# Kernel optimization log

Hardware: AMD Instinct MI355X
Metric: run time of the kernel (lower is better)

## Reference

```python
import jax, jax.numpy as jnp
import numpy as np

B, N, E, H = 4, 8192, 256, 8
EXP = 4  # params['num_layers'] -> MLP expansion
HID = EXP * E
EPS = 1e-5


def _layernorm(x, w, b):
    mu = jnp.mean(x, axis=-1, keepdims=True)
    var = jnp.mean(jnp.square(x - mu), axis=-1, keepdims=True)
    return (x - mu) * jax.lax.rsqrt(var + EPS) * w + b


def _mish(x):
    return x * jnp.tanh(jax.nn.softplus(x))


def setup_inputs() -> dict:
    key = jax.random.key(0)
    ks = jax.random.split(key, 12)
    s = 0.02
    return {
        "x": jax.random.normal(ks[0], (B, N, E), dtype=jnp.float32),
        "ln1_w": jnp.ones((E,), jnp.float32),
        "ln1_b": jnp.zeros((E,), jnp.float32),
        "Wq": jax.random.normal(ks[1], (E, E), jnp.float32) * s,
        "bq": jnp.zeros((E,), jnp.float32),
        "Wk": jax.random.normal(ks[2], (E, E), jnp.float32) * s,
        "bk": jnp.zeros((E,), jnp.float32),
        "Wv": jax.random.normal(ks[3], (E, E), jnp.float32) * s,
        "bv": jnp.zeros((E,), jnp.float32),
        "Wp": jax.random.normal(ks[4], (E, E), jnp.float32) * s,
        "bp": jnp.zeros((E,), jnp.float32),
        "ln2_w": jnp.ones((E,), jnp.float32),
        "ln2_b": jnp.zeros((E,), jnp.float32),
        "W1": jax.random.normal(ks[5], (HID, E), jnp.float32) * s,
        "b1": jnp.zeros((HID,), jnp.float32),
        "W2": jax.random.normal(ks[6], (E, HID), jnp.float32) * s,
        "b2": jnp.zeros((E,), jnp.float32),
    }


def _msa(x, Wq, bq, Wk, bk, Wv, bv, Wp, bp):
    b, n, e = x.shape
    d = n // H  # sequence-chunk per head (faithful to source rearrange)
    q = (x @ Wq.T + bq).reshape(b, H, d, e)
    k = (x @ Wk.T + bk).reshape(b, H, d, e)
    v = (x @ Wv.T + bv).reshape(b, H, d, e)
    scale = jnp.sqrt(jnp.float32(E))
    energy = jnp.einsum('bhie,bhke->bhik', q, k)  # (b,H,d,d)
    att = jax.nn.softmax(energy, axis=3) / scale
    o = jnp.einsum('bhik,bhke->bhie', att, v).reshape(b, n, e)
    return o @ Wp.T + bp


def reference(x, ln1_w, ln1_b, Wq, bq, Wk, bk, Wv, bv, Wp, bp,
              ln2_w, ln2_b, W1, b1, W2, b2):
    # pre-LN attention block + residual
    x1 = _msa(_layernorm(x, ln1_w, ln1_b), Wq, bq, Wk, bk, Wv, bv, Wp, bp) + x
    # pre-LN MLP (Mish after both linears, per source) + residual
    h = _layernorm(x1, ln2_w, ln2_b)
    h = _mish(h @ W1.T + b1)
    h = _mish(h @ W2.T + b2)
    return h + x1
```

## Files before the change

kernel.cpp:

```cpp
#include <hip/hip_runtime.h>

typedef float  f32x4  __attribute__((ext_vector_type(4)));
typedef float  f4v    __attribute__((ext_vector_type(4)));
typedef __bf16 bf16x8 __attribute__((ext_vector_type(8)));
typedef __bf16 bf16x4 __attribute__((ext_vector_type(4)));
typedef unsigned short ushort_t;

#define AS1 __attribute__((address_space(1)))
#define AS3 __attribute__((address_space(3)))

static __device__ __forceinline__ void gload_lds16(const void* g, void* l) {
  __builtin_amdgcn_global_load_lds((const AS1 void*)g, (AS3 void*)l, 16, 0, 0);
}

static __device__ __forceinline__ float mishf(float x) {
  float t = __expf(x);
  float u = t * (t + 2.f);
  float y = x * __fdividef(u, u + 2.f);
  return (x > 15.f) ? x : y;
}

__global__ __launch_bounds__(256) void packw(
    const float* __restrict__ Wq, const float* __restrict__ Wk,
    const float* __restrict__ Wv, const float* __restrict__ Wp,
    const float* __restrict__ W1, const float* __restrict__ W2,
    __bf16* __restrict__ out)
{
  const int t = blockIdx.x * 256 + threadIdx.x;
  const int e0 = t * 8;
  int rel, K; const float* src;
  if      (e0 < 196608) { rel = e0;          K = 256;  src = nullptr; }
  else if (e0 < 262144) { rel = e0 - 196608; K = 256;  src = Wp; }
  else if (e0 < 524288) { rel = e0 - 262144; K = 256;  src = W1; }
  else                  { rel = e0 - 524288; K = 1024; src = W2; }
  const int percb = (K >> 8) * 8192;
  const int cb = rel / percb;  const int r1 = rel % percb;
  const int c  = r1 / 8192;    const int r2 = r1 % 8192;
  const int u  = r2 / 1024;    const int r3 = r2 % 1024;
  const int n  = r3 / 512;     const int l  = (r3 % 512) >> 3;
  const int col = cb * 32 + n * 16 + (l & 15);
  const int k   = c * 256 + u * 32 + ((l >> 4) << 3);
  const float* sp;
  if (e0 < 196608) {
    const float* qkvsrc = (col < 256) ? Wq : (col < 512 ? Wk : Wv);
    sp = qkvsrc + (size_t)(col & 255) * 256 + k;
  } else {
    sp = src + (size_t)col * K + k;
  }
  const f4v a = *(const f4v*)(sp);
  const f4v b = *(const f4v*)(sp + 4);
  bf16x8 o;
  #pragma unroll
  for (int j = 0; j < 4; ++j) { o[j] = (__bf16)a[j]; o[4 + j] = (__bf16)b[j]; }
  *(bf16x8*)(out + e0) = o;
}

__global__ void packb(const float* __restrict__ a, const float* __restrict__ b,
                      const float* __restrict__ c, float* __restrict__ o) {
  int i = threadIdx.x;
  o[i] = (i < 256) ? a[i] : (i < 512 ? b[i - 256] : c[i - 512]);
}

__global__ __launch_bounds__(256) void ln_rows(
    const float* __restrict__ X, const float* __restrict__ g,
    const float* __restrict__ b, __bf16* __restrict__ Y)
{
  const int l = threadIdx.x & 63;
  const size_t row = (size_t)blockIdx.x * 4 + (threadIdx.x >> 6);
  const f4v x = *(const f4v*)(X + row * 256 + l * 4);
  float s = x[0] + x[1] + x[2] + x[3];
  float q = x[0]*x[0] + x[1]*x[1] + x[2]*x[2] + x[3]*x[3];
  #pragma unroll
  for (int d = 1; d < 64; d <<= 1) { s += __shfl_xor(s, d); q += __shfl_xor(q, d); }
  const float mu = s * (1.f / 256.f);
  const float rs = rsqrtf(q * (1.f / 256.f) - mu * mu + 1e-5f);
  const f4v gv = *(const f4v*)(g + l * 4);
  const f4v bv = *(const f4v*)(b + l * 4);
  bf16x4 o;
  #pragma unroll
  for (int j = 0; j < 4; ++j) o[j] = (__bf16)((x[j] - mu) * rs * gv[j] + bv[j]);
  *(bf16x4*)(Y + row * 256 + l * 4) = o;
}

template<int BM, int NT, int KC, int ACT, int RES, int OUTBF>
__global__ __launch_bounds__(512, 2) void bgemm(
    const __bf16* __restrict__ A, const __bf16* __restrict__ Wg,
    const float* __restrict__ bias, const float* __restrict__ res,
    void* __restrict__ out, int ldo)
{
  constexpr int K  = KC * 256;
  constexpr int MR = BM / 32;
  __shared__ __bf16 Ab[BM * 256];
  const int tid = threadIdx.x, l = tid & 63, w = tid >> 6;
  const int wr = w >> 2, wc = w & 3;
  constexpr int nwg = (32768 / BM) * NT;
  const int wg = (blockIdx.x & 7) * (nwg / 8) + (blockIdx.x >> 3);
  const int mt = wg / NT, nt = wg % NT;
  const int row0 = mt * BM;
  const int col0 = nt * 256 + wc * 64;
  const int cb0 = nt * 8 + wc * 2;

  auto stageA = [&](int c) {
    #pragma unroll
    for (int j = 0; j < BM / 16; ++j) {
      const int s = j * 512 + tid;
      const int r = s >> 5, q = s & 31;
      gload_lds16(A + (size_t)(row0 + r) * K + c * 256 + ((q ^ (r & 7)) << 3),
                  &Ab[s << 3]);
    }
  };

  auto ldBu = [&](bf16x8* d, int c, int u) {
    const __bf16* wp0 = Wg + ((size_t)cb0 * KC + c) * 8192 + (((u << 1) * 64 + l) << 3);
    const __bf16* wp1 = wp0 + (size_t)KC * 8192;
    d[0] = *(const bf16x8*)(wp0);
    d[1] = *(const bf16x8*)(wp0 + 512);
    d[2] = *(const bf16x8*)(wp1);
    d[3] = *(const bf16x8*)(wp1 + 512);
  };

  f32x4 acc[MR][4] = {};

  stageA(0);
  asm volatile("s_waitcnt vmcnt(0)" ::: "memory");
  __builtin_amdgcn_s_barrier();

  for (int c = 0;;) {
    bf16x8 b0[4], b1[4];
    ldBu(b0, c, 0);
    #pragma unroll
    for (int u = 0; u < 8; ++u) {
      if (u + 1 < 8) ldBu((u & 1) ? b0 : b1, c, u + 1);
      const bf16x8* bu = (u & 1) ? b1 : b0;
      bf16x8 af[MR];
      #pragma unroll
      for (int m = 0; m < MR; ++m) {
        const int r = wr * (BM / 2) + m * 16 + (l & 15);
        const int q = ((u << 2) | (l >> 4)) ^ (r & 7);
        af[m] = *(const bf16x8*)&Ab[((r << 5) | q) << 3];
      }
      #pragma unroll
      for (int m = 0; m < MR; ++m)
        #pragma unroll
        for (int n = 0; n < 4; ++n)
          acc[m][n] = __builtin_amdgcn_mfma_f32_16x16x32_bf16(af[m], bu[n], acc[m][n], 0, 0, 0);
    }
    if (++c == KC) break;
    __syncthreads();
    stageA(c);
    asm volatile("s_waitcnt vmcnt(0)" ::: "memory");
    __builtin_amdgcn_s_barrier();
  }

  float bs[4];
  #pragma unroll
  for (int n = 0; n < 4; ++n) bs[n] = bias[col0 + n * 16 + (l & 15)];
  #pragma unroll
  for (int m = 0; m < MR; ++m) {
    #pragma unroll
    for (int r = 0; r < 4; ++r) {
      const int row = row0 + wr * (BM / 2) + m * 16 + ((l >> 4) << 2) + r;
      float v[4];
      #pragma unroll
      for (int n = 0; n < 4; ++n) {
        v[n] = acc[m][n][r] + bs[n];
        if (ACT) v[n] = mishf(v[n]);
      }
      if (OUTBF) {
        __bf16* op = (__bf16*)out + (size_t)row * ldo + col0;
        #pragma unroll
        for (int n = 0; n < 4; ++n) op[n * 16 + (l & 15)] = (__bf16)v[n];
      } else {
        float* op = (float*)out + (size_t)row * ldo + col0;
        if (RES) {
          const float* rp = res + (size_t)row * ldo + col0;
          #pragma unroll
          for (int n = 0; n < 4; ++n) v[n] += rp[n * 16 + (l & 15)];
        }
        #pragma unroll
        for (int n = 0; n < 4; ++n) op[n * 16 + (l & 15)] = v[n];
      }
    }
  }
}

__global__ __launch_bounds__(512) void attn_fwd(
    const __bf16* __restrict__ QKV, __bf16* __restrict__ Om)
{
  __shared__ __bf16 Ks[2][32][256];
  __shared__ __bf16 Vs[2][256][32];
  __shared__ __bf16 Ps[8][16][32];
  const int tid = threadIdx.x, l = tid & 63, w = tid >> 6;
  const int wgs = (blockIdx.x & 7) * 32 + (blockIdx.x >> 3);
  const int bh = wgs >> 3, qt = wgs & 7;
  const size_t rbase = (size_t)bh * 1024 * 768;
  const int qr0 = qt * 128 + w * 16;

  bf16x8 qf[8];
  {
    const __bf16* qp = QKV + rbase + (size_t)(qr0 + (l & 15)) * 768 + ((l >> 4) << 3);
    #pragma unroll
    for (int s = 0; s < 8; ++s) qf[s] = *(const bf16x8*)(qp + s * 32);
  }
  f32x4 acc[16] = {};
  float lacc[4] = {0.f, 0.f, 0.f, 0.f};

  const int kec = tid & 31, kr_ = tid >> 5;
  const int vp = tid & 15, vc = tid >> 4;
  const __bf16* gK = QKV + 256 + rbase + kec * 8;
  const __bf16* gV = QKV + 512 + rbase + vc * 8;

  uint4 rk0, rk1, rv0, rv1;
  auto ldKV = [&](int kt) {
    const __bf16* k0 = gK + (size_t)(kt * 32 + kr_) * 768;
    rk0 = *(const uint4*)k0;
    rk1 = *(const uint4*)(k0 + 16 * 768);
    const __bf16* v0 = gV + (size_t)(kt * 32 + vp * 2) * 768;
    rv0 = *(const uint4*)v0;
    rv1 = *(const uint4*)(v0 + 768);
  };
  auto wrKV = [&](int buf) {
    char* kb = (char*)&Ks[buf][0][0];
    const int a0 = (kr_ * 512 + kec * 16) ^ ((kr_ & 15) << 4);
    const int a1 = ((kr_ + 16) * 512 + kec * 16) ^ (((kr_ + 16) & 15) << 4);
    *(uint4*)(kb + a0) = rk0;
    *(uint4*)(kb + a1) = rk1;
    const ushort_t* s0 = (const ushort_t*)&rv0;
    const ushort_t* s1 = (const ushort_t*)&rv1;
    #pragma unroll
    for (int i = 0; i < 8; ++i) {
      unsigned pk = (unsigned)s0[i] | ((unsigned)s1[i] << 16);
      *(unsigned*)&Vs[buf][vc * 8 + i][vp * 2] = pk;
    }
  };

  ldKV(0); wrKV(0);
  __syncthreads();
  int cur = 0;
  for (int kt = 0;;) {
    if (kt + 1 < 32) ldKV(kt + 1);
    f32x4 S[2] = {};
    const char* kbase = (const char*)&Ks[cur][0][0];
    #pragma unroll
    for (int t = 0; t < 2; ++t) {
      const int kcol = t * 16 + (l & 15);
      const int swz = (kcol & 15) << 4;
      #pragma unroll
      for (int s = 0; s < 8; ++s) {
        uint4 kf = *(const uint4*)(kbase + ((kcol * 512 + s * 64 + ((l >> 4) << 4)) ^ swz));
        S[t] = __builtin_amdgcn_mfma_f32_16x16x32_bf16(qf[s], __builtin_bit_cast(bf16x8, kf), S[t], 0, 0, 0);
      }
    }
    #pragma unroll
    for (int t = 0; t < 2; ++t)
      #pragma unroll
      for (int r = 0; r < 4; ++r) {
        float p = __expf(S[t][r]);
        lacc[r] += p;
        Ps[w][((l >> 4) << 2) + r][t * 16 + (l & 15)] = (__bf16)p;
      }
    bf16x8 pf = *(const bf16x8*)&Ps[w][l & 15][(l >> 4) << 3];
    #pragma unroll
    for (int n = 0; n < 16; ++n) {
      uint4 vf = *(const uint4*)&Vs[cur][n * 16 + (l & 15)][(l >> 4) << 3];
      acc[n] = __builtin_amdgcn_mfma_f32_16x16x32_bf16(pf, __builtin_bit_cast(bf16x8, vf), acc[n], 0, 0, 0);
    }
    if (++kt == 32) break;
    wrKV(cur ^ 1);
    __syncthreads();
    cur ^= 1;
  }
  f32x4 inv;
  #pragma unroll
  for (int r = 0; r < 4; ++r) {
    float s = lacc[r];
    s += __shfl_xor(s, 1); s += __shfl_xor(s, 2);
    s += __shfl_xor(s, 4); s += __shfl_xor(s, 8);
    inv[r] = 1.f / (16.f * s);
  }
  __bf16* op = Om + (size_t)(bh * 1024 + qr0 + ((l >> 4) << 2)) * 256 + (l & 15);
  #pragma unroll
  for (int n = 0; n < 16; ++n)
    #pragma unroll
    for (int r = 0; r < 4; ++r)
      op[(size_t)r * 256 + n * 16] = (__bf16)(acc[n][r] * inv[r]);
}

extern "C" void kernel_launch(void* const* d_in, const int* in_sizes, int n_in,
                              void* d_out, int out_size, void* d_ws, size_t ws_size,
                              hipStream_t stream)
{
  const float* x    = (const float*)d_in[0];
  const float* ln1w = (const float*)d_in[1];
  const float* ln1b = (const float*)d_in[2];
  const float* Wq   = (const float*)d_in[3];
  const float* bq   = (const float*)d_in[4];
  const float* Wk   = (const float*)d_in[5];
  const float* bk   = (const float*)d_in[6];
  const float* Wv   = (const float*)d_in[7];
  const float* bv   = (const float*)d_in[8];
  const float* Wp   = (const float*)d_in[9];
  const float* bp   = (const float*)d_in[10];
  const float* ln2w = (const float*)d_in[11];
  const float* ln2b = (const float*)d_in[12];
  const float* W1   = (const float*)d_in[13];
  const float* b1   = (const float*)d_in[14];
  const float* W2   = (const float*)d_in[15];
  const float* b2   = (const float*)d_in[16];

  char* ws = (char*)d_ws;
  __bf16* wb   = (__bf16*)(ws);
  float*  bqkv = (float*)(ws + 1572864);
  __bf16* y    = (__bf16*)(ws + 2097152);
  __bf16* qkv  = (__bf16*)(ws + 18874368);
  float*  x1   = (float*)(ws + 18874368);
  __bf16* hb   = (__bf16*)(ws + 52428800);
  __bf16* h1   = (__bf16*)(ws + 69206016);
  __bf16* ao   = y;
  float*  outp = (float*)d_out;

  packw<<<384, 256, 0, stream>>>(Wq, Wk, Wv, Wp, W1, W2, wb);
  packb<<<1, 768, 0, stream>>>(bq, bk, bv, bqkv);
  ln_rows<<<8192, 256, 0, stream>>>(x, ln1w, ln1b, y);
  bgemm<128, 3, 1, 0, 0, 1><<<768,  512, 0, stream>>>(y,  wb,          bqkv, nullptr, qkv,  768);
  attn_fwd<<<256, 512, 0, stream>>>(qkv, ao);
  bgemm<64, 1, 1, 0, 1, 0><<<512,  512, 0, stream>>>(ao, wb + 196608, bp,   x,       x1,   256);
  ln_rows<<<8192, 256, 0, stream>>>(x1, ln2w, ln2b, hb);
  bgemm<128, 4, 1, 1, 0, 1><<<1024, 512, 0, stream>>>(hb, wb + 262144, b1,  nullptr, h1,  1024);
  bgemm<64, 1, 4, 1, 1, 0><<<512,  512, 0, stream>>>(h1, wb + 524288, b2,   x1,      outp, 256);
}
```

Measured before the change: 204.0 us.

## Fuse both LayerNorms into adjacent GEMMs and store residual x1 in bf16

LN1 is now computed in the QKV GEMM's A-staging step, which reads fp32 x directly and writes normalized bf16 into LDS. LN2 is fused into the projection GEMM's epilogue, with row statistics reduced across waves through shared memory. That epilogue writes both the residual x1 and the normalized hb. x1 is now stored in bf16, which halves its write and reread traffic in the final GEMM. This removes two standalone LN launches and their round trips through memory. The cost is lower precision in the residual path and synchronous, non-async A staging for the QKV GEMM.

```diff
diff --git a/kernel.cpp b/kernel.cpp
--- a/kernel.cpp
+++ b/kernel.cpp
@@ -61,36 +61,20 @@
   o[i] = (i < 256) ? a[i] : (i < 512 ? b[i - 256] : c[i - 512]);
 }
 
-__global__ __launch_bounds__(256) void ln_rows(
-    const float* __restrict__ X, const float* __restrict__ g,
-    const float* __restrict__ b, __bf16* __restrict__ Y)
-{
-  const int l = threadIdx.x & 63;
-  const size_t row = (size_t)blockIdx.x * 4 + (threadIdx.x >> 6);
-  const f4v x = *(const f4v*)(X + row * 256 + l * 4);
-  float s = x[0] + x[1] + x[2] + x[3];
-  float q = x[0]*x[0] + x[1]*x[1] + x[2]*x[2] + x[3]*x[3];
-  #pragma unroll
-  for (int d = 1; d < 64; d <<= 1) { s += __shfl_xor(s, d); q += __shfl_xor(q, d); }
-  const float mu = s * (1.f / 256.f);
-  const float rs = rsqrtf(q * (1.f / 256.f) - mu * mu + 1e-5f);
-  const f4v gv = *(const f4v*)(g + l * 4);
-  const f4v bv = *(const f4v*)(b + l * 4);
-  bf16x4 o;
-  #pragma unroll
-  for (int j = 0; j < 4; ++j) o[j] = (__bf16)((x[j] - mu) * rs * gv[j] + bv[j]);
-  *(bf16x4*)(Y + row * 256 + l * 4) = o;
-}
-
-template<int BM, int NT, int KC, int ACT, int RES, int OUTBF>
+template<int BM, int NT, int KC, int ACT, int RES, int OUTBF,
+         int LNSTAGE, int LNFUSE, int RESBF>
 __global__ __launch_bounds__(512, 2) void bgemm(
-    const __bf16* __restrict__ A, const __bf16* __restrict__ Wg,
-    const float* __restrict__ bias, const float* __restrict__ res,
-    void* __restrict__ out, int ldo)
+    const __bf16* __restrict__ A, const float* __restrict__ Xf,
+    const __bf16* __restrict__ Wg, const float* __restrict__ bias,
+    const void* __restrict__ res, const float* __restrict__ lnw,
+    const float* __restrict__ lnb, void* __restrict__ out,
+    void* __restrict__ out2, int ldo)
 {
   constexpr int K  = KC * 256;
   constexpr int MR = BM / 32;
   __shared__ __bf16 Ab[BM * 256];
+  __shared__ float redS[64][4];
+  __shared__ float redQ[64][4];
   const int tid = threadIdx.x, l = tid & 63, w = tid >> 6;
   const int wr = w >> 2, wc = w & 3;
   constexpr int nwg = (32768 / BM) * NT;
@@ -121,9 +105,41 @@
 
   f32x4 acc[MR][4] = {};
 
-  stageA(0);
-  asm volatile("s_waitcnt vmcnt(0)" ::: "memory");
-  __builtin_amdgcn_s_barrier();
+  if constexpr (LNSTAGE) {
+    const int q = tid & 31;
+    const f4v ga0 = *(const f4v*)(lnw + q * 8);
+    const f4v ga1 = *(const f4v*)(lnw + q * 8 + 4);
+    const f4v bb0 = *(const f4v*)(lnb + q * 8);
+    const f4v bb1 = *(const f4v*)(lnb + q * 8 + 4);
+    #pragma unroll
+    for (int j = 0; j < BM / 16; ++j) {
+      const int s = j * 512 + tid, r = s >> 5;
+      const float* xp = Xf + (size_t)(row0 + r) * 256 + q * 8;
+      const f4v xa = *(const f4v*)xp;
+      const f4v xb = *(const f4v*)(xp + 4);
+      float s1 = xa[0] + xa[1] + xa[2] + xa[3] + xb[0] + xb[1] + xb[2] + xb[3];
+      float s2 = xa[0]*xa[0] + xa[1]*xa[1] + xa[2]*xa[2] + xa[3]*xa[3]
+               + xb[0]*xb[0] + xb[1]*xb[1] + xb[2]*xb[2] + xb[3]*xb[3];
+      #pragma unroll
+      for (int mk = 1; mk < 32; mk <<= 1) {
+        s1 += __shfl_xor(s1, mk); s2 += __shfl_xor(s2, mk);
+      }
+      const float mu = s1 * (1.f / 256.f);
+      const float rs = rsqrtf(s2 * (1.f / 256.f) - mu * mu + 1e-5f);
+      bf16x8 o;
+      #pragma unroll
+      for (int i = 0; i < 4; ++i) {
+        o[i]     = (__bf16)((xa[i] - mu) * rs * ga0[i] + bb0[i]);
+        o[4 + i] = (__bf16)((xb[i] - mu) * rs * ga1[i] + bb1[i]);
+      }
+      *(bf16x8*)&Ab[((r << 5) | (q ^ (r & 7))) << 3] = o;
+    }
+    __syncthreads();
+  } else {
+    stageA(0);
+    asm volatile("s_waitcnt vmcnt(0)" ::: "memory");
+    __builtin_amdgcn_s_barrier();
+  }
 
   for (int c = 0;;) {
     bf16x8 b0[4], b1[4];
@@ -155,30 +171,88 @@
   float bs[4];
   #pragma unroll
   for (int n = 0; n < 4; ++n) bs[n] = bias[col0 + n * 16 + (l & 15)];
-  #pragma unroll
-  for (int m = 0; m < MR; ++m) {
-    #pragma unroll
-    for (int r = 0; r < 4; ++r) {
-      const int row = row0 + wr * (BM / 2) + m * 16 + ((l >> 4) << 2) + r;
-      float v[4];
-      #pragma unroll
-      for (int n = 0; n < 4; ++n) {
-        v[n] = acc[m][n][r] + bs[n];
-        if (ACT) v[n] = mishf(v[n]);
-      }
-      if (OUTBF) {
-        __bf16* op = (__bf16*)out + (size_t)row * ldo + col0;
+
+  if constexpr (LNFUSE) {
+    #pragma unroll
+    for (int m = 0; m < MR; ++m) {
+      #pragma unroll
+      for (int r = 0; r < 4; ++r) {
+        const int row = row0 + wr * (BM / 2) + m * 16 + ((l >> 4) << 2) + r;
+        const float* rp = (const float*)res + (size_t)row * ldo + col0;
+        float s1v = 0.f, s2v = 0.f;
         #pragma unroll
-        for (int n = 0; n < 4; ++n) op[n * 16 + (l & 15)] = (__bf16)v[n];
-      } else {
-        float* op = (float*)out + (size_t)row * ldo + col0;
+        for (int n = 0; n < 4; ++n) {
+          float v = acc[m][n][r] + bs[n] + rp[n * 16 + (l & 15)];
+          acc[m][n][r] = v;
+          s1v += v; s2v += v * v;
+        }
+        #pragma unroll
+        for (int mk = 1; mk < 16; mk <<= 1) {
+          s1v += __shfl_xor(s1v, mk); s2v += __shfl_xor(s2v, mk);
+        }
+        if ((l & 15) == 0) { redS[row - row0][wc] = s1v; redQ[row - row0][wc] = s2v; }
+      }
+    }
+    __syncthreads();
+    float wlv[4], blv[4];
+    #pragma unroll
+    for (int n = 0; n < 4; ++n) {
+      wlv[n] = lnw[col0 + n * 16 + (l & 15)];
+      blv[n] = lnb[col0 + n * 16 + (l & 15)];
+    }
+    #pragma unroll
+    for (int m = 0; m < MR; ++m) {
+      #pragma unroll
+      for (int r = 0; r < 4; ++r) {
+        const int row = row0 + wr * (BM / 2) + m * 16 + ((l >> 4) << 2) + r;
+        const int lrow = row - row0;
+        const f4v ss = *(const f4v*)redS[lrow];
+        const f4v qq = *(const f4v*)redQ[lrow];
+        const float mu = (ss[0] + ss[1] + ss[2] + ss[3]) * (1.f / 256.f);
+        const float var = (qq[0] + qq[1] + qq[2] + qq[3]) * (1.f / 256.f) - mu * mu;
+        const float rsv = rsqrtf(var + 1e-5f);
+        __bf16* o1 = (__bf16*)out  + (size_t)row * ldo + col0;
+        __bf16* o2 = (__bf16*)out2 + (size_t)row * ldo + col0;
+        #pragma unroll
+        for (int n = 0; n < 4; ++n) {
+          const float v = acc[m][n][r];
+          o1[n * 16 + (l & 15)] = (__bf16)v;
+          o2[n * 16 + (l & 15)] = (__bf16)((v - mu) * rsv * wlv[n] + blv[n]);
+        }
+      }
+    }
+  } else {
+    #pragma unroll
+    for (int m = 0; m < MR; ++m) {
+      #pragma unroll
+      for (int r = 0; r < 4; ++r) {
+        const int row = row0 + wr * (BM / 2) + m * 16 + ((l >> 4) << 2) + r;
+        float v[4];
+        #pragma unroll
+        for (int n = 0; n < 4; ++n) {
+          v[n] = acc[m][n][r] + bs[n];
+          if (ACT) v[n] = mishf(v[n]);
+        }
         if (RES) {
-          const float* rp = res + (size_t)row * ldo + col0;
+          if constexpr (RESBF) {
+            const __bf16* rp = (const __bf16*)res + (size_t)row * ldo + col0;
+            #pragma unroll
+            for (int n = 0; n < 4; ++n) v[n] += (float)rp[n * 16 + (l & 15)];
+          } else {
+            const float* rp = (const float*)res + (size_t)row * ldo + col0;
+            #pragma unroll
+            for (int n = 0; n < 4; ++n) v[n] += rp[n * 16 + (l & 15)];
+          }
+        }
+        if (OUTBF) {
+          __bf16* op = (__bf16*)out + (size_t)row * ldo + col0;
           #pragma unroll
-          for (int n = 0; n < 4; ++n) v[n] += rp[n * 16 + (l & 15)];
-        }
-        #pragma unroll
-        for (int n = 0; n < 4; ++n) op[n * 16 + (l & 15)] = v[n];
+          for (int n = 0; n < 4; ++n) op[n * 16 + (l & 15)] = (__bf16)v[n];
+        } else {
+          float* op = (float*)out + (size_t)row * ldo + col0;
+          #pragma unroll
+          for (int n = 0; n < 4; ++n) op[n * 16 + (l & 15)] = v[n];
+        }
       }
     }
   }
@@ -313,7 +387,7 @@
   float*  bqkv = (float*)(ws + 1572864);
   __bf16* y    = (__bf16*)(ws + 2097152);
   __bf16* qkv  = (__bf16*)(ws + 18874368);
-  float*  x1   = (float*)(ws + 18874368);
+  __bf16* x1b  = (__bf16*)(ws + 18874368);
   __bf16* hb   = (__bf16*)(ws + 52428800);
   __bf16* h1   = (__bf16*)(ws + 69206016);
   __bf16* ao   = y;
@@ -321,11 +395,13 @@
 
   packw<<<384, 256, 0, stream>>>(Wq, Wk, Wv, Wp, W1, W2, wb);
   packb<<<1, 768, 0, stream>>>(bq, bk, bv, bqkv);
-  ln_rows<<<8192, 256, 0, stream>>>(x, ln1w, ln1b, y);
-  bgemm<128, 3, 1, 0, 0, 1><<<768,  512, 0, stream>>>(y,  wb,          bqkv, nullptr, qkv,  768);
+  bgemm<128, 3, 1, 0, 0, 1, 1, 0, 0><<<768, 512, 0, stream>>>(
+      nullptr, x, wb, bqkv, nullptr, ln1w, ln1b, qkv, nullptr, 768);
   attn_fwd<<<256, 512, 0, stream>>>(qkv, ao);
-  bgemm<64, 1, 1, 0, 1, 0><<<512,  512, 0, stream>>>(ao, wb + 196608, bp,   x,       x1,   256);
-  ln_rows<<<8192, 256, 0, stream>>>(x1, ln2w, ln2b, hb);
-  bgemm<128, 4, 1, 1, 0, 1><<<1024, 512, 0, stream>>>(hb, wb + 262144, b1,  nullptr, h1,  1024);
-  bgemm<64, 1, 4, 1, 1, 0><<<512,  512, 0, stream>>>(h1, wb + 524288, b2,   x1,      outp, 256);
-}
+  bgemm<64, 1, 1, 0, 1, 0, 0, 1, 0><<<512, 512, 0, stream>>>(
+      ao, nullptr, wb + 196608, bp, x, ln2w, ln2b, x1b, hb, 256);
+  bgemm<128, 4, 1, 1, 0, 1, 0, 0, 0><<<1024, 512, 0, stream>>>(
+      hb, nullptr, wb + 262144, b1, nullptr, nullptr, nullptr, h1, nullptr, 1024);
+  bgemm<64, 1, 4, 1, 1, 0, 0, 0, 1><<<512, 512, 0, stream>>>(
+      h1, nullptr, wb + 524288, b2, x1b, nullptr, nullptr, outp, nullptr, 256);
+}
```

After: 196.0 us. 1.04x faster.
